# Performance work log

Measured on AMD Instinct MI355X. Metric: run time of the kernel, lower is better.

## Reference

```python
import jax, jax.numpy as jnp
import numpy as np

B, C, H, W_SP = 4, 64, 64, 64
CI = C // 2  # inter_channels = 32
DEPTH = 64
EPS = 1e-5


def conv2d(x, w, b, pad=0, dil=1):
    out = jax.lax.conv_general_dilated(
        x, w, window_strides=(1, 1),
        padding=[(pad, pad), (pad, pad)],
        rhs_dilation=(dil, dil),
        dimension_numbers=('NCHW', 'OIHW', 'NCHW'))
    return out + b[None, :, None, None]


def setup_inputs() -> dict:
    key = jax.random.key(0)
    ks = iter(jax.random.split(key, 32))
    nrm = lambda shp, s=0.01: jax.random.normal(next(ks), shp, jnp.float32) * s
    inp = {
        'x': jax.random.normal(next(ks), (B, C, H, W_SP), jnp.float32),
        # NonlocalBlock params (init: normal(0, 0.01), bias 0)
        'g_w': nrm((CI, C, 1, 1)), 'g_b': jnp.zeros((CI,), jnp.float32),
        'theta_w': nrm((CI, C, 1, 1)), 'theta_b': jnp.zeros((CI,), jnp.float32),
        'phi_w': nrm((CI, C, 1, 1)), 'phi_b': jnp.zeros((CI,), jnp.float32),
        'Wz_w': nrm((C, CI, 1, 1)), 'Wz_b': jnp.zeros((C,), jnp.float32),
        'bn_g': jax.random.normal(next(ks), (C,), jnp.float32),  # normal_(W[1].weight, 0) -> std 1
        'bn_b': jnp.zeros((C,), jnp.float32),
        # ASPP params (torch default kaiming init approximated by small normals)
        'a_mean_w': nrm((DEPTH, C, 1, 1), 0.05), 'a_mean_b': jnp.zeros((DEPTH,), jnp.float32),
        'a1_w': nrm((DEPTH, C, 1, 1), 0.05), 'a1_b': jnp.zeros((DEPTH,), jnp.float32),
        'a3_w': nrm((DEPTH, C, 3, 3), 0.02), 'a3_b': jnp.zeros((DEPTH,), jnp.float32),
        'a5_w': nrm((DEPTH, C, 3, 3), 0.02), 'a5_b': jnp.zeros((DEPTH,), jnp.float32),
        'a7_w': nrm((DEPTH, C, 3, 3), 0.02), 'a7_b': jnp.zeros((DEPTH,), jnp.float32),
        'out_w': nrm((DEPTH, DEPTH * 5, 1, 1), 0.02), 'out_b': jnp.zeros((DEPTH,), jnp.float32),
    }
    return inp


def _forward(x, g_w, g_b, theta_w, theta_b, phi_w, phi_b, Wz_w, Wz_b, bn_g, bn_b,
             a_mean_w, a_mean_b, a1_w, a1_b, a3_w, a3_b, a5_w, a5_b, a7_w, a7_b,
             out_w, out_b):
    b, c, h, w = x.shape
    n = h * w
    # ---- NonlocalBlock: global self-attention ----
    g_x = conv2d(x, g_w, g_b).reshape(b, CI, n).transpose(0, 2, 1)       # [B,N,Ci]
    theta_x = conv2d(x, theta_w, theta_b).reshape(b, CI, n).transpose(0, 2, 1)  # [B,N,Ci]
    phi_x = conv2d(x, phi_w, phi_b).reshape(b, CI, n)                    # [B,Ci,N]
    f = jnp.einsum('bqc,bck->bqk', theta_x, phi_x)                       # [B,N,N]
    f_div_C = jax.nn.softmax(f, axis=2)
    y = jnp.einsum('bqk,bkc->bqc', f_div_C, g_x)                         # [B,N,Ci]
    y = y.transpose(0, 2, 1).reshape(b, CI, h, w)
    wy = conv2d(y, Wz_w, Wz_b)
    # BatchNorm (eval: running_mean=0, running_var=1)
    wy = wy * (bn_g / jnp.sqrt(1.0 + EPS))[None, :, None, None] + bn_b[None, :, None, None]
    z = wy + x
    # ---- ASPP ----
    img = jnp.mean(z, axis=(2, 3), keepdims=True)                        # [B,C,1,1]
    img = conv2d(img, a_mean_w, a_mean_b)                                # [B,D,1,1]
    img = jnp.broadcast_to(img, (b, DEPTH, h, w))  # bilinear upsample of 1x1 is constant
    b1 = conv2d(z, a1_w, a1_b)
    b3 = conv2d(z, a3_w, a3_b, pad=3, dil=3)
    b5 = conv2d(z, a5_w, a5_b, pad=5, dil=5)
    b7 = conv2d(z, a7_w, a7_b, pad=7, dil=7)
    cat = jnp.concatenate([img, b1, b3, b5, b7], axis=1)                 # [B,5D,H,W]
    return conv2d(cat, out_w, out_b)                                     # [B,D,H,W]


def reference(x, g_w, g_b, theta_w, theta_b, phi_w, phi_b, Wz_w, Wz_b, bn_g, bn_b,
              a_mean_w, a_mean_b, a1_w, a1_b, a3_w, a3_b, a5_w, a5_b, a7_w, a7_b,
              out_w, out_b):
    return _forward(x, g_w, g_b, theta_w, theta_b, phi_w, phi_b, Wz_w, Wz_b, bn_g, bn_b,
                    a_mean_w, a_mean_b, a1_w, a1_b, a3_w, a3_b, a5_w, a5_b, a7_w, a7_b,
                    out_w, out_b)
```

## Files before the change

### kernel.cpp

```cpp
#include <hip/hip_runtime.h>


typedef __attribute__((ext_vector_type(8))) short bf16x8;
typedef __attribute__((ext_vector_type(4))) short s16x4;
typedef __attribute__((ext_vector_type(4))) float f32x4;

#define MFMA(a, b, c) __builtin_amdgcn_mfma_f32_16x16x32_bf16((a), (b), (c), 0, 0, 0)

#if __has_builtin(__builtin_amdgcn_exp2f)
#define EXP2(x) __builtin_amdgcn_exp2f(x)
#else
#define EXP2(x) exp2f(x)
#endif

__device__ static inline short f2bf(float f) {
  union { float f; unsigned u; } v; v.f = f;
  unsigned r = v.u + 0x7fffu + ((v.u >> 16) & 1u);
  return (short)(r >> 16);
}
__device__ static inline s16x4 pk4(f32x4 v) {
  s16x4 r; r.x = f2bf(v.x); r.y = f2bf(v.y); r.z = f2bf(v.z); r.w = f2bf(v.w);
  return r;
}
__device__ static inline unsigned pk2(float f0, float f1) {
  union { float f; unsigned u; } a, b; a.f = f0; b.f = f1;
  return __builtin_amdgcn_perm(b.u, a.u, 0x07060302u);
}
__device__ static inline float unlo(unsigned d) {
  union { unsigned u; float f; } v; v.u = d << 16; return v.f;
}
__device__ static inline float unhi(unsigned d) {
  union { unsigned u; float f; } v; v.u = d & 0xffff0000u; return v.f;
}
__device__ static inline unsigned fasu(float f) {
  union { float f; unsigned u; } v; v.f = f; return v.u;
}
__device__ static inline float uasf(unsigned u) {
  union { unsigned u; float f; } v; v.u = u; return v.f;
}
__device__ static inline f32x4 exp24(f32x4 v) {
  f32x4 r; r.x = EXP2(v.x); r.y = EXP2(v.y); r.z = EXP2(v.z); r.w = EXP2(v.w);
  return r;
}

#define QF_PER_B 131072
#define ZPB      389376
#define LOG2E    1.4426950408889634f

__global__ __launch_bounds__(256) void k_proj(
    const float* __restrict__ x,
    const float* __restrict__ tw, const float* __restrict__ tb,
    const float* __restrict__ pw, const float* __restrict__ pb,
    const float* __restrict__ gw, const float* __restrict__ gb,
    const float* __restrict__ Wz_w, const float* __restrict__ Wz_b,
    const float* __restrict__ bn_g, const float* __restrict__ bn_b,
    const float* __restrict__ out_w, const float* __restrict__ out_b,
    const float* __restrict__ a1_w, const float* __restrict__ a3_w,
    const float* __restrict__ a5_w, const float* __restrict__ a7_w,
    const float* __restrict__ a1_b, const float* __restrict__ a3_b,
    const float* __restrict__ a5_b, const float* __restrict__ a7_b,
    const float* __restrict__ am_w,
    unsigned short* __restrict__ thetaB, unsigned short* __restrict__ phiB,
    unsigned short* __restrict__ gB, unsigned short* __restrict__ WzF,
    float* __restrict__ bias2, float* __restrict__ zmean,
    unsigned* __restrict__ zp, unsigned short* __restrict__ Wfrag,
    float* __restrict__ am_wT, float* __restrict__ owT0,
    float* __restrict__ cbias) {
  __shared__ union {
    struct { float wl[2048]; float bl[32]; } qkv;
    struct { float wsm[4096]; float osm[64 * 65]; } prep;
  } sm;
  int blk = blockIdx.x, t = threadIdx.x;
  if (blk < 192) {
    int b = blk & 3, pt = (blk >> 2) & 15, proj = blk >> 6;
    const float* w    = proj == 0 ? tw : (proj == 1 ? pw : gw);
    const float* bias = proj == 0 ? tb : (proj == 1 ? pb : gb);
    for (int i = t; i < 2048; i += 256) sm.qkv.wl[i] = w[i];
    if (t < 32) sm.qkv.bl[t] = bias[t];
    __syncthreads();
    int pix = pt*256 + t;
    const float* xp = x + b*64*4096 + pix;
    float acc[32];
    #pragma unroll
    for (int ci = 0; ci < 32; ++ci) acc[ci] = sm.qkv.bl[ci];
    for (int c0 = 0; c0 < 64; c0 += 16) {
      float xv[16];
      #pragma unroll
      for (int k = 0; k < 16; ++k) xv[k] = xp[(c0 + k)*4096];
      #pragma unroll
      for (int k = 0; k < 16; ++k)
        #pragma unroll
        for (int ci = 0; ci < 32; ++ci) acc[ci] += sm.qkv.wl[ci*64 + c0 + k] * xv[k];
    }
    if (proj == 0) {
      #pragma unroll
      for (int ci = 0; ci < 32; ++ci) acc[ci] *= LOG2E;
    }
    if (proj < 2) {
      unsigned short* base = (proj == 0 ? thetaB : phiB) + b*QF_PER_B
                             + (pix >> 4)*512 + (pix & 15)*8;
      #pragma unroll
      for (int q = 0; q < 4; ++q) {
        bf16x8 v;
        #pragma unroll
        for (int j = 0; j < 8; ++j) v[j] = f2bf(acc[q*8 + j]);
        *(bf16x8*)(base + q*128) = v;
      }
    } else {
      unsigned short* base = gB + b*QF_PER_B + (pix >> 5)*1024
                             + ((pix & 31) >> 3)*128 + (pix & 7);
      #pragma unroll
      for (int ci = 0; ci < 32; ++ci)
        base[(ci >> 4)*512 + (ci & 15)*8] = (unsigned short)f2bf(acc[ci]);
    }
  } else if (blk == 192) {
    int ct = t >> 6, lane = t & 63, quad = lane >> 4, l15 = lane & 15;
    int c = ct * 16 + l15;
    float s = bn_g[c] * rsqrtf(1.f + 1e-5f);
    bf16x8 v;
    #pragma unroll
    for (int j = 0; j < 8; ++j) v[j] = f2bf(s * Wz_w[c * 32 + quad * 8 + j]);
    *(bf16x8*)(WzF + (ct * 64 + lane) * 8) = v;
    zmean[t] = 0.f;
    if (t < 64) {
      float s2 = bn_g[t] * rsqrtf(1.f + 1e-5f);
      bias2[t] = s2 * Wz_b[t] + bn_b[t];
    }
  } else if (blk < 1189) {
    int hb = blk - 193;
    int b = hb / 249, loc = hb - b * 249;
    int i = loc * 256 + t;
    if (i >= 63616) return;
    int px = i >> 5, dw = i & 31;
    int row, col;
    if (px < 1092) {
      int r = px / 78; col = px - r * 78;
      row = (r < 7) ? r : r + 64;
    } else {
      int j = px - 1092;
      int r = j / 14; int c = j - r * 14;
      row = r + 7; col = (c < 7) ? c : c + 64;
    }
    zp[b * (ZPB / 2) + (row * 78 + col) * 32 + dw] = 0u;
  } else if (blk < 1217) {
    int tap = blk - 1189;
    const float* w; int goff, kyx = 0, ksq = 9;
    if (tap == 0)      { w = a1_w; goff = 64;  ksq = 1; }
    else if (tap < 10) { w = a3_w; goff = 128; kyx = tap - 1; }
    else if (tap < 19) { w = a5_w; goff = 192; kyx = tap - 10; }
    else               { w = a7_w; goff = 256; kyx = tap - 19; }
    for (int i = t; i < 4096; i += 256) {
      sm.prep.wsm[i] = w[i * ksq + kyx];
      int d = i >> 6, m = i & 63;
      sm.prep.osm[d * 65 + m] = out_w[d * 320 + goff + m];
    }
    __syncthreads();
    int dt = t >> 6, lane = t & 63, quad = lane >> 4, l15 = lane & 15;
    int d = dt * 16 + l15;
    float acc[16];
    #pragma unroll
    for (int k = 0; k < 16; ++k) acc[k] = 0.f;
    const float* orow = sm.prep.osm + d * 65;
    int c0 = quad * 8;
    for (int m = 0; m < 64; ++m) {
      float o = orow[m];
      const float* wr = sm.prep.wsm + m * 64 + c0;
      #pragma unroll
      for (int cc = 0; cc < 2; ++cc)
        #pragma unroll
        for (int j = 0; j < 8; ++j)
          acc[cc * 8 + j] += o * wr[cc * 32 + j];
    }
    #pragma unroll
    for (int cc = 0; cc < 2; ++cc) {
      bf16x8 v;
      #pragma unroll
      for (int j = 0; j < 8; ++j) v[j] = f2bf(acc[cc * 8 + j]);
      *(bf16x8*)(Wfrag + (((tap * 4 + dt) * 2 + cc) * 64 + lane) * 8) = v;
    }
  } else {
    for (int i = t; i < 4096; i += 256) {
      int d = i >> 6, c = i & 63;
      am_wT[c * 64 + d] = am_w[i];
      owT0[c * 64 + d] = out_w[d * 320 + c];
    }
    if (t < 64) {
      float r = out_b[t];
      const float* ow = out_w + t * 320;
      for (int m = 0; m < 64; ++m)
        r += ow[64 + m] * a1_b[m] + ow[128 + m] * a3_b[m]
           + ow[192 + m] * a5_b[m] + ow[256 + m] * a7_b[m];
      cbias[t] = r;
    }
  }
}

__global__ __launch_bounds__(512, 4) void k_attn(
    const unsigned short* __restrict__ thetaB, const unsigned short* __restrict__ phiB,
    const unsigned short* __restrict__ gB, const unsigned short* __restrict__ WzF,
    const float* __restrict__ bias2, const float* __restrict__ x,
    unsigned short* __restrict__ z_pad, float* __restrict__ zmean) {
  __shared__ struct {
    unsigned ypk[8][10][64];
    __align__(16) unsigned short plds[8][1152];
  } sm;
  int blk = blockIdx.x;
  int b = blk >> 7, qblk = blk & 127;
  int tid = threadIdx.x;
  int kh = tid >> 6, lane = tid & 63, quad = lane >> 4, l15 = lane & 15;
  const bf16x8* thB = (const bf16x8*)(thetaB + b*QF_PER_B);
  const bf16x8* phF = (const bf16x8*)(phiB + b*QF_PER_B);
  const bf16x8* gF  = (const bf16x8*)(gB + b*QF_PER_B);
  bf16x8 th0 = thB[(qblk*2 + 0)*64 + lane];
  bf16x8 th1 = thB[(qblk*2 + 1)*64 + lane];
  bf16x8 ones;
  #pragma unroll
  for (int j = 0; j < 8; ++j) ones[j] = (short)0x3F80;
  const f32x4 z4 = {0.f, 0.f, 0.f, 0.f};
  f32x4 acc00 = z4, acc01 = z4, acc10 = z4, acc11 = z4;
  f32x4 accL0 = z4, accL1 = z4;
  unsigned short* pl = &sm.plds[kh][0];
  unsigned short* r0p = pl + l15*36 + quad*4;
  unsigned short* r1p = pl + 576 + l15*36 + quad*4;
  const unsigned short* q0p = pl + l15*36 + quad*8;
  const unsigned short* q1p = pl + 576 + l15*36 + quad*8;
  int kt0 = kh*16;
  int tb0 = kt0*128 + lane;
  bf16x8 pf0 = phF[tb0], pf1 = phF[tb0 + 64];
  bf16x8 gf0 = gF[tb0],  gf1 = gF[tb0 + 64];
  for (int kt = kt0; kt < kt0 + 16; ++kt) {
    bf16x8 cp0 = pf0, cp1 = pf1, cg0 = gf0, cg1 = gf1;
    if (kt + 1 < kt0 + 16) {
      int tb = (kt + 1)*128 + lane;
      pf0 = phF[tb]; pf1 = phF[tb + 64];
      gf0 = gF[tb];  gf1 = gF[tb + 64];
    }
    f32x4 s00 = MFMA(cp0, th0, z4);
    f32x4 s10 = MFMA(cp1, th0, z4);
    f32x4 s01 = MFMA(cp0, th1, z4);
    f32x4 s11 = MFMA(cp1, th1, z4);
    f32x4 p00 = exp24(s00), p10 = exp24(s10), p01 = exp24(s01), p11 = exp24(s11);
    uint2 w0; w0.x = pk2(p00.x, p00.y); w0.y = pk2(p00.z, p00.w);
    uint2 w1; w1.x = pk2(p10.x, p10.y); w1.y = pk2(p10.z, p10.w);
    uint2 w2; w2.x = pk2(p01.x, p01.y); w2.y = pk2(p01.z, p01.w);
    uint2 w3; w3.x = pk2(p11.x, p11.y); w3.y = pk2(p11.z, p11.w);
    *(uint2*)(r0p)      = w0;
    *(uint2*)(r0p + 16) = w1;
    *(uint2*)(r1p)      = w2;
    *(uint2*)(r1p + 16) = w3;
    uint2 a0 = *(const uint2*)(q0p);
    uint2 a1 = *(const uint2*)(q0p + 4);
    uint2 b0 = *(const uint2*)(q1p);
    uint2 b1 = *(const uint2*)(q1p + 4);
    union { unsigned u[4]; bf16x8 v; } pb0c, pb1c;
    pb0c.u[0] = a0.x; pb0c.u[1] = a0.y; pb0c.u[2] = a1.x; pb0c.u[3] = a1.y;
    pb1c.u[0] = b0.x; pb1c.u[1] = b0.y; pb1c.u[2] = b1.x; pb1c.u[3] = b1.y;
    acc00 = MFMA(cg0, pb0c.v, acc00);
    acc01 = MFMA(cg1, pb0c.v, acc01);
    acc10 = MFMA(cg0, pb1c.v, acc10);
    acc11 = MFMA(cg1, pb1c.v, acc11);
    accL0 = MFMA(ones, pb0c.v, accL0);
    accL1 = MFMA(ones, pb1c.v, accL1);
  }
  {
    unsigned* yp = &sm.ypk[kh][0][lane];
    yp[0*64] = pk2(acc00.x, acc00.y);
    yp[1*64] = pk2(acc00.z, acc00.w);
    yp[2*64] = pk2(acc01.x, acc01.y);
    yp[3*64] = pk2(acc01.z, acc01.w);
    yp[4*64] = pk2(acc10.x, acc10.y);
    yp[5*64] = pk2(acc10.z, acc10.w);
    yp[6*64] = pk2(acc11.x, acc11.y);
    yp[7*64] = pk2(acc11.z, acc11.w);
    yp[8*64] = fasu(accL0.x);
    yp[9*64] = fasu(accL1.x);
  }
  __syncthreads();
  if (kh >= 4) return;
  int ct = kh;
  f32x4 a00 = z4, a01 = z4, a10 = z4, a11 = z4;
  float l0 = 0.f, l1 = 0.f;
  #pragma unroll
  for (int k = 0; k < 8; ++k) {
    const unsigned* q = &sm.ypk[k][0][lane];
    unsigned d0v = q[0], d1v = q[64], d2v = q[128], d3v = q[192];
    unsigned d4v = q[256], d5v = q[320], d6v = q[384], d7v = q[448];
    a00.x += unlo(d0v); a00.y += unhi(d0v); a00.z += unlo(d1v); a00.w += unhi(d1v);
    a01.x += unlo(d2v); a01.y += unhi(d2v); a01.z += unlo(d3v); a01.w += unhi(d3v);
    a10.x += unlo(d4v); a10.y += unhi(d4v); a10.z += unlo(d5v); a10.w += unhi(d5v);
    a11.x += unlo(d6v); a11.y += unhi(d6v); a11.z += unlo(d7v); a11.w += unhi(d7v);
    l0 += uasf(q[512]); l1 += uasf(q[576]);
  }
  float r0 = 1.f / l0, r1 = 1.f / l1;
  a00 *= r0; a01 *= r0; a10 *= r1; a11 *= r1;
  unsigned short* yl = &sm.plds[0][0] + ct*1280;
  *(s16x4*)(yl + l15*40 + quad*4)             = pk4(a00);
  *(s16x4*)(yl + l15*40 + 16 + quad*4)        = pk4(a01);
  *(s16x4*)(yl + (16 + l15)*40 + quad*4)      = pk4(a10);
  *(s16x4*)(yl + (16 + l15)*40 + 16 + quad*4) = pk4(a11);
  bf16x8 y0 = *(const bf16x8*)(yl + l15*40 + quad*8);
  bf16x8 y1 = *(const bf16x8*)(yl + (16 + l15)*40 + quad*8);
  bf16x8 wf = ((const bf16x8*)WzF)[ct*64 + lane];
  f32x4 zq0 = MFMA(wf, y0, z4);
  f32x4 zq1 = MFMA(wf, y1, z4);
  int c0 = ct*16 + quad*4;
  f32x4 b2 = *(const f32x4*)(bias2 + c0);
  int q0i = qblk * 32;
  const float* xp0 = x + (b*64 + c0)*4096 + q0i + l15;
  f32x4 s0, s1;
  s0.x = zq0.x + b2.x + xp0[0];
  s0.y = zq0.y + b2.y + xp0[4096];
  s0.z = zq0.z + b2.z + xp0[8192];
  s0.w = zq0.w + b2.w + xp0[12288];
  s1.x = zq1.x + b2.x + xp0[16];
  s1.y = zq1.y + b2.y + xp0[4096 + 16];
  s1.z = zq1.z + b2.z + xp0[8192 + 16];
  s1.w = zq1.w + b2.w + xp0[12288 + 16];
  {
    int q = q0i + l15, h = q >> 6, w = q & 63;
    *(s16x4*)(z_pad + b*ZPB + ((h + 7)*78 + (w + 7))*64 + c0) = pk4(s0);
    q = q0i + 16 + l15; h = q >> 6; w = q & 63;
    *(s16x4*)(z_pad + b*ZPB + ((h + 7)*78 + (w + 7))*64 + c0) = pk4(s1);
  }
  f32x4 zs = s0 + s1;
  #pragma unroll
  for (int m = 1; m < 16; m <<= 1) {
    zs.x += __shfl_xor(zs.x, m);
    zs.y += __shfl_xor(zs.y, m);
    zs.z += __shfl_xor(zs.z, m);
    zs.w += __shfl_xor(zs.w, m);
  }
  if (l15 == 0) {
    atomicAdd(zmean + b*64 + c0 + 0, zs.x);
    atomicAdd(zmean + b*64 + c0 + 1, zs.y);
    atomicAdd(zmean + b*64 + c0 + 2, zs.z);
    atomicAdd(zmean + b*64 + c0 + 3, zs.w);
  }
}

__global__ __launch_bounds__(256, 4) void k_conv(
    const unsigned short* __restrict__ z_pad, const unsigned short* __restrict__ Wfrag,
    const float* __restrict__ zmean, const float* __restrict__ am_wT,
    const float* __restrict__ am_b, const float* __restrict__ owT0,
    const float* __restrict__ cbias, float* __restrict__ out) {
  static constexpr int DYt[28] = {0, -3,-3,-3,0,0,0,3,3,3,
                                     -5,-5,-5,0,0,0,5,5,5,
                                     -7,-7,-7,0,0,0,7,7,7};
  static constexpr int DXt[28] = {0, -3,0,3,-3,0,3,-3,0,3,
                                     -5,0,5,-5,0,5,-5,0,5,
                                     -7,0,7,-7,0,7,-7,0,7};
  int blk = blockIdx.x;
  int b = blk >> 6, h = blk & 63;
  int tid = threadIdx.x;
  int wave = tid >> 6, lane = tid & 63, quad = lane >> 4, l15 = lane & 15;
  int dt2 = wave >> 1, wt2 = wave & 1;
  float zml = zmean[b*64 + lane] * (1.f / 4096.f);
  float img = am_b[lane];
  for (int c = 0; c < 64; ++c) img += am_wT[c*64 + lane] * __shfl(zml, c);
  float cbd = cbias[lane];
  for (int dd = 0; dd < 64; ++dd) cbd += owT0[dd*64 + lane] * __shfl(img, dd);
  const unsigned short* zb = z_pad + b*ZPB + ((h + 7)*78 + 7)*64 + quad*8;
  const bf16x8* wfp = (const bf16x8*)Wfrag + lane;
  int d0 = dt2*2 + 0, d1 = dt2*2 + 1;
  const f32x4 z4 = {0.f, 0.f, 0.f, 0.f};
  f32x4 acc00 = z4, acc01 = z4, acc10 = z4, acc11 = z4;
  int col0 = ((wt2*2 + 0)*16 + l15)*64;
  int col1 = ((wt2*2 + 1)*16 + l15)*64;
  bf16x8 zq0[4], zq1[4], wq0[4], wq1[4];
  #pragma unroll
  for (int p = 0; p < 4; ++p) {
    int tap = p >> 1, cc = p & 1;
    const unsigned short* nz = zb + (DYt[tap]*78 + DXt[tap])*64 + cc*32;
    zq0[p] = *(const bf16x8*)(nz + col0);
    zq1[p] = *(const bf16x8*)(nz + col1);
    wq0[p] = wfp[((tap*4 + d0)*2 + cc)*64];
    wq1[p] = wfp[((tap*4 + d1)*2 + cc)*64];
  }
  #pragma unroll
  for (int idx = 0; idx < 56; ++idx) {
    int slot = idx & 3;
    bf16x8 zc0 = zq0[slot], zc1 = zq1[slot], wc0 = wq0[slot], wc1 = wq1[slot];
    if (idx + 4 < 56) {
      int ntap = (idx + 4) >> 1, ncc = (idx + 4) & 1;
      const unsigned short* nz = zb + (DYt[ntap]*78 + DXt[ntap])*64 + ncc*32;
      zq0[slot] = *(const bf16x8*)(nz + col0);
      zq1[slot] = *(const bf16x8*)(nz + col1);
      wq0[slot] = wfp[((ntap*4 + d0)*2 + ncc)*64];
      wq1[slot] = wfp[((ntap*4 + d1)*2 + ncc)*64];
    }
    acc00 = MFMA(wc0, zc0, acc00);
    acc01 = MFMA(wc0, zc1, acc01);
    acc10 = MFMA(wc1, zc0, acc10);
    acc11 = MFMA(wc1, zc1, acc11);
  }
  int dd0 = d0*16 + quad*4, dd1 = d1*16 + quad*4;
  f32x4 cb0v, cb1v;
  cb0v.x = __shfl(cbd, dd0 + 0); cb0v.y = __shfl(cbd, dd0 + 1);
  cb0v.z = __shfl(cbd, dd0 + 2); cb0v.w = __shfl(cbd, dd0 + 3);
  cb1v.x = __shfl(cbd, dd1 + 0); cb1v.y = __shfl(cbd, dd1 + 1);
  cb1v.z = __shfl(cbd, dd1 + 2); cb1v.w = __shfl(cbd, dd1 + 3);
  acc00 += cb0v; acc01 += cb0v; acc10 += cb1v; acc11 += cb1v;
  float* ob = out + b*262144 + h*64;
  int w0 = (wt2*2 + 0)*16 + l15, w1 = (wt2*2 + 1)*16 + l15;
  ob[(dd0 + 0)*4096 + w0] = acc00.x;
  ob[(dd0 + 1)*4096 + w0] = acc00.y;
  ob[(dd0 + 2)*4096 + w0] = acc00.z;
  ob[(dd0 + 3)*4096 + w0] = acc00.w;
  ob[(dd0 + 0)*4096 + w1] = acc01.x;
  ob[(dd0 + 1)*4096 + w1] = acc01.y;
  ob[(dd0 + 2)*4096 + w1] = acc01.z;
  ob[(dd0 + 3)*4096 + w1] = acc01.w;
  ob[(dd1 + 0)*4096 + w0] = acc10.x;
  ob[(dd1 + 1)*4096 + w0] = acc10.y;
  ob[(dd1 + 2)*4096 + w0] = acc10.z;
  ob[(dd1 + 3)*4096 + w0] = acc10.w;
  ob[(dd1 + 0)*4096 + w1] = acc11.x;
  ob[(dd1 + 1)*4096 + w1] = acc11.y;
  ob[(dd1 + 2)*4096 + w1] = acc11.z;
  ob[(dd1 + 3)*4096 + w1] = acc11.w;
}

extern "C" void kernel_launch(void* const* d_in, const int* in_sizes, int n_in,
                              void* d_out, int out_size, void* d_ws, size_t ws_size,
                              hipStream_t stream) {
  const float* x    = (const float*)d_in[0];
  const float* g_w  = (const float*)d_in[1];
  const float* g_b  = (const float*)d_in[2];
  const float* th_w = (const float*)d_in[3];
  const float* th_b = (const float*)d_in[4];
  const float* ph_w = (const float*)d_in[5];
  const float* ph_b = (const float*)d_in[6];
  const float* Wz_w = (const float*)d_in[7];
  const float* Wz_b = (const float*)d_in[8];
  const float* bn_g = (const float*)d_in[9];
  const float* bn_b = (const float*)d_in[10];
  const float* am_w = (const float*)d_in[11];
  const float* am_b = (const float*)d_in[12];
  const float* a1_w = (const float*)d_in[13];
  const float* a1_b = (const float*)d_in[14];
  const float* a3_w = (const float*)d_in[15];
  const float* a3_b = (const float*)d_in[16];
  const float* a5_w = (const float*)d_in[17];
  const float* a5_b = (const float*)d_in[18];
  const float* a7_w = (const float*)d_in[19];
  const float* a7_b = (const float*)d_in[20];
  const float* out_w = (const float*)d_in[21];
  const float* out_b = (const float*)d_in[22];
  float* out = (float*)d_out;
  char* ws = (char*)d_ws;
  unsigned short* thetaB = (unsigned short*)(ws + 0);
  unsigned short* phiB   = (unsigned short*)(ws + 1048576);
  unsigned short* gB     = (unsigned short*)(ws + 2097152);
  unsigned short* z_pad  = (unsigned short*)(ws + 3145728);
  unsigned short* Wfrag  = (unsigned short*)(ws + 6260736);
  unsigned short* WzF    = (unsigned short*)(ws + 6490112);
  float* zmean           = (float*)(ws + 6494208);
  float* bias2           = (float*)(ws + 6495232);
  float* am_wT           = (float*)(ws + 6495488);
  float* owT0            = (float*)(ws + 6511872);
  float* cbias           = (float*)(ws + 6528256);

  k_proj<<<dim3(1218), dim3(256), 0, stream>>>(
      x, th_w, th_b, ph_w, ph_b, g_w, g_b, Wz_w, Wz_b, bn_g, bn_b,
      out_w, out_b, a1_w, a3_w, a5_w, a7_w, a1_b, a3_b, a5_b, a7_b, am_w,
      thetaB, phiB, gB, WzF, bias2, zmean,
      (unsigned*)z_pad, Wfrag, am_wT, owT0, cbias);
  k_attn<<<dim3(512), dim3(512), 0, stream>>>(thetaB, phiB, gB, WzF, bias2, x,
                                              z_pad, zmean);
  k_conv<<<dim3(256), dim3(256), 0, stream>>>(z_pad, Wfrag, zmean, am_wT, am_b,
                                              owT0, cbias, out);
}
```

Before: 180.7 us.

## Halve per-block work across all three kernels and add XCD-aware block mapping

Doubles the grid of each kernel by splitting work. The projection kernel splits output channels across two thread halves and reads weights from LDS as transposed vector loads. Attention handles 16 queries per block with launch bounds raised to 8, and conv handles 32 columns per block. Attention and conv blocks are remapped so blocks on the same XCD share a batch or rows for L2 locality. The z-mean accumulation is spread over 8 partial buffers to reduce atomic contention. The trade-off is less register reuse per block: theta and weights are reloaded more often, and gB loads are no longer prefetched.

```diff
diff --git a/kernel.cpp b/kernel.cpp
--- a/kernel.cpp
+++ b/kernel.cpp
@@ -62,58 +62,68 @@
     const float* __restrict__ am_w,
     unsigned short* __restrict__ thetaB, unsigned short* __restrict__ phiB,
     unsigned short* __restrict__ gB, unsigned short* __restrict__ WzF,
-    float* __restrict__ bias2, float* __restrict__ zmean,
+    float* __restrict__ bias2, float* __restrict__ zpart,
     unsigned* __restrict__ zp, unsigned short* __restrict__ Wfrag,
     float* __restrict__ am_wT, float* __restrict__ owT0,
     float* __restrict__ cbias) {
   __shared__ union {
-    struct { float wl[2048]; float bl[32]; } qkv;
+    struct { float wlT[2048]; float bl[32]; } qkv;
     struct { float wsm[4096]; float osm[64 * 65]; } prep;
   } sm;
   int blk = blockIdx.x, t = threadIdx.x;
-  if (blk < 192) {
-    int b = blk & 3, pt = (blk >> 2) & 15, proj = blk >> 6;
+  if (blk < 384) {
+    int proj = blk >> 7, r = blk & 127;
+    int b = r & 3, pt = r >> 2;
     const float* w    = proj == 0 ? tw : (proj == 1 ? pw : gw);
     const float* bias = proj == 0 ? tb : (proj == 1 ? pb : gb);
-    for (int i = t; i < 2048; i += 256) sm.qkv.wl[i] = w[i];
+    for (int i = t; i < 2048; i += 256)
+      sm.qkv.wlT[(i & 63) * 32 + (i >> 6)] = w[i];
     if (t < 32) sm.qkv.bl[t] = bias[t];
     __syncthreads();
-    int pix = pt*256 + t;
-    const float* xp = x + b*64*4096 + pix;
-    float acc[32];
+    int px = pt * 128 + (t & 127), tci = t >> 7;
+    const float* xp = x + b*64*4096 + px;
+    float acc[16];
     #pragma unroll
-    for (int ci = 0; ci < 32; ++ci) acc[ci] = sm.qkv.bl[ci];
+    for (int i = 0; i < 16; ++i) acc[i] = sm.qkv.bl[tci*16 + i];
     for (int c0 = 0; c0 < 64; c0 += 16) {
       float xv[16];
       #pragma unroll
       for (int k = 0; k < 16; ++k) xv[k] = xp[(c0 + k)*4096];
       #pragma unroll
-      for (int k = 0; k < 16; ++k)
+      for (int k = 0; k < 16; ++k) {
+        const float* wr = &sm.qkv.wlT[(c0 + k)*32 + tci*16];
         #pragma unroll
-        for (int ci = 0; ci < 32; ++ci) acc[ci] += sm.qkv.wl[ci*64 + c0 + k] * xv[k];
+        for (int j = 0; j < 4; ++j) {
+          f32x4 wv = *(const f32x4*)(wr + j*4);
+          acc[j*4 + 0] += wv.x * xv[k];
+          acc[j*4 + 1] += wv.y * xv[k];
+          acc[j*4 + 2] += wv.z * xv[k];
+          acc[j*4 + 3] += wv.w * xv[k];
+        }
+      }
     }
     if (proj == 0) {
       #pragma unroll
-      for (int ci = 0; ci < 32; ++ci) acc[ci] *= LOG2E;
+      for (int i = 0; i < 16; ++i) acc[i] *= LOG2E;
     }
     if (proj < 2) {
       unsigned short* base = (proj == 0 ? thetaB : phiB) + b*QF_PER_B
-                             + (pix >> 4)*512 + (pix & 15)*8;
-      #pragma unroll
-      for (int q = 0; q < 4; ++q) {
+                             + (px >> 4)*512 + (px & 15)*8;
+      #pragma unroll
+      for (int qq = 0; qq < 2; ++qq) {
         bf16x8 v;
         #pragma unroll
-        for (int j = 0; j < 8; ++j) v[j] = f2bf(acc[q*8 + j]);
-        *(bf16x8*)(base + q*128) = v;
+        for (int j = 0; j < 8; ++j) v[j] = f2bf(acc[qq*8 + j]);
+        *(bf16x8*)(base + (tci*2 + qq)*128) = v;
       }
     } else {
-      unsigned short* base = gB + b*QF_PER_B + (pix >> 5)*1024
-                             + ((pix & 31) >> 3)*128 + (pix & 7);
-      #pragma unroll
-      for (int ci = 0; ci < 32; ++ci)
-        base[(ci >> 4)*512 + (ci & 15)*8] = (unsigned short)f2bf(acc[ci]);
-    }
-  } else if (blk == 192) {
+      unsigned short* base = gB + b*QF_PER_B + (px >> 5)*1024
+                             + ((px & 31) >> 3)*128 + (px & 7) + tci*512;
+      #pragma unroll
+      for (int ci = 0; ci < 16; ++ci)
+        base[ci*8] = (unsigned short)f2bf(acc[ci]);
+    }
+  } else if (blk == 384) {
     int ct = t >> 6, lane = t & 63, quad = lane >> 4, l15 = lane & 15;
     int c = ct * 16 + l15;
     float s = bn_g[c] * rsqrtf(1.f + 1e-5f);
@@ -121,13 +131,14 @@
     #pragma unroll
     for (int j = 0; j < 8; ++j) v[j] = f2bf(s * Wz_w[c * 32 + quad * 8 + j]);
     *(bf16x8*)(WzF + (ct * 64 + lane) * 8) = v;
-    zmean[t] = 0.f;
+    #pragma unroll
+    for (int i = 0; i < 8; ++i) zpart[i*256 + t] = 0.f;
     if (t < 64) {
       float s2 = bn_g[t] * rsqrtf(1.f + 1e-5f);
       bias2[t] = s2 * Wz_b[t] + bn_b[t];
     }
-  } else if (blk < 1189) {
-    int hb = blk - 193;
+  } else if (blk < 1381) {
+    int hb = blk - 385;
     int b = hb / 249, loc = hb - b * 249;
     int i = loc * 256 + t;
     if (i >= 63616) return;
@@ -142,8 +153,8 @@
       row = r + 7; col = (c < 7) ? c : c + 64;
     }
     zp[b * (ZPB / 2) + (row * 78 + col) * 32 + dw] = 0u;
-  } else if (blk < 1217) {
-    int tap = blk - 1189;
+  } else if (blk < 1409) {
+    int tap = blk - 1381;
     const float* w; int goff, kyx = 0, ksq = 9;
     if (tap == 0)      { w = a1_w; goff = 64;  ksq = 1; }
     else if (tap < 10) { w = a3_w; goff = 128; kyx = tap - 1; }
@@ -195,134 +206,100 @@
   }
 }
 
-__global__ __launch_bounds__(512, 4) void k_attn(
+__global__ __launch_bounds__(512, 8) void k_attn(
     const unsigned short* __restrict__ thetaB, const unsigned short* __restrict__ phiB,
     const unsigned short* __restrict__ gB, const unsigned short* __restrict__ WzF,
     const float* __restrict__ bias2, const float* __restrict__ x,
-    unsigned short* __restrict__ z_pad, float* __restrict__ zmean) {
+    unsigned short* __restrict__ z_pad, float* __restrict__ zpart) {
   __shared__ struct {
-    unsigned ypk[8][10][64];
-    __align__(16) unsigned short plds[8][1152];
+    unsigned ypk[8][5][64];
+    __align__(16) unsigned short plds[8][576];
   } sm;
   int blk = blockIdx.x;
-  int b = blk >> 7, qblk = blk & 127;
+  int xcd = blk & 7;
+  int b = xcd >> 1;
+  int qblk = ((xcd & 1) << 7) | (blk >> 3);
   int tid = threadIdx.x;
   int kh = tid >> 6, lane = tid & 63, quad = lane >> 4, l15 = lane & 15;
   const bf16x8* thB = (const bf16x8*)(thetaB + b*QF_PER_B);
   const bf16x8* phF = (const bf16x8*)(phiB + b*QF_PER_B);
   const bf16x8* gF  = (const bf16x8*)(gB + b*QF_PER_B);
-  bf16x8 th0 = thB[(qblk*2 + 0)*64 + lane];
-  bf16x8 th1 = thB[(qblk*2 + 1)*64 + lane];
+  bf16x8 th = thB[qblk*64 + lane];
   bf16x8 ones;
   #pragma unroll
   for (int j = 0; j < 8; ++j) ones[j] = (short)0x3F80;
   const f32x4 z4 = {0.f, 0.f, 0.f, 0.f};
-  f32x4 acc00 = z4, acc01 = z4, acc10 = z4, acc11 = z4;
-  f32x4 accL0 = z4, accL1 = z4;
+  f32x4 acc0 = z4, acc1 = z4, accL = z4;
   unsigned short* pl = &sm.plds[kh][0];
-  unsigned short* r0p = pl + l15*36 + quad*4;
-  unsigned short* r1p = pl + 576 + l15*36 + quad*4;
-  const unsigned short* q0p = pl + l15*36 + quad*8;
-  const unsigned short* q1p = pl + 576 + l15*36 + quad*8;
+  unsigned short* rp = pl + l15*36 + quad*4;
+  const unsigned short* qp = pl + l15*36 + quad*8;
   int kt0 = kh*16;
   int tb0 = kt0*128 + lane;
   bf16x8 pf0 = phF[tb0], pf1 = phF[tb0 + 64];
-  bf16x8 gf0 = gF[tb0],  gf1 = gF[tb0 + 64];
   for (int kt = kt0; kt < kt0 + 16; ++kt) {
-    bf16x8 cp0 = pf0, cp1 = pf1, cg0 = gf0, cg1 = gf1;
+    bf16x8 cp0 = pf0, cp1 = pf1;
+    bf16x8 gf0 = gF[kt*128 + lane];
+    bf16x8 gf1 = gF[kt*128 + lane + 64];
     if (kt + 1 < kt0 + 16) {
       int tb = (kt + 1)*128 + lane;
       pf0 = phF[tb]; pf1 = phF[tb + 64];
-      gf0 = gF[tb];  gf1 = gF[tb + 64];
-    }
-    f32x4 s00 = MFMA(cp0, th0, z4);
-    f32x4 s10 = MFMA(cp1, th0, z4);
-    f32x4 s01 = MFMA(cp0, th1, z4);
-    f32x4 s11 = MFMA(cp1, th1, z4);
-    f32x4 p00 = exp24(s00), p10 = exp24(s10), p01 = exp24(s01), p11 = exp24(s11);
-    uint2 w0; w0.x = pk2(p00.x, p00.y); w0.y = pk2(p00.z, p00.w);
-    uint2 w1; w1.x = pk2(p10.x, p10.y); w1.y = pk2(p10.z, p10.w);
-    uint2 w2; w2.x = pk2(p01.x, p01.y); w2.y = pk2(p01.z, p01.w);
-    uint2 w3; w3.x = pk2(p11.x, p11.y); w3.y = pk2(p11.z, p11.w);
-    *(uint2*)(r0p)      = w0;
-    *(uint2*)(r0p + 16) = w1;
-    *(uint2*)(r1p)      = w2;
-    *(uint2*)(r1p + 16) = w3;
-    uint2 a0 = *(const uint2*)(q0p);
-    uint2 a1 = *(const uint2*)(q0p + 4);
-    uint2 b0 = *(const uint2*)(q1p);
-    uint2 b1 = *(const uint2*)(q1p + 4);
-    union { unsigned u[4]; bf16x8 v; } pb0c, pb1c;
-    pb0c.u[0] = a0.x; pb0c.u[1] = a0.y; pb0c.u[2] = a1.x; pb0c.u[3] = a1.y;
-    pb1c.u[0] = b0.x; pb1c.u[1] = b0.y; pb1c.u[2] = b1.x; pb1c.u[3] = b1.y;
-    acc00 = MFMA(cg0, pb0c.v, acc00);
-    acc01 = MFMA(cg1, pb0c.v, acc01);
-    acc10 = MFMA(cg0, pb1c.v, acc10);
-    acc11 = MFMA(cg1, pb1c.v, acc11);
-    accL0 = MFMA(ones, pb0c.v, accL0);
-    accL1 = MFMA(ones, pb1c.v, accL1);
+    }
+    f32x4 s0 = MFMA(cp0, th, z4);
+    f32x4 s1 = MFMA(cp1, th, z4);
+    f32x4 p0 = exp24(s0), p1 = exp24(s1);
+    uint2 w0; w0.x = pk2(p0.x, p0.y); w0.y = pk2(p0.z, p0.w);
+    uint2 w1; w1.x = pk2(p1.x, p1.y); w1.y = pk2(p1.z, p1.w);
+    *(uint2*)(rp)      = w0;
+    *(uint2*)(rp + 16) = w1;
+    uint2 a0 = *(const uint2*)(qp);
+    uint2 a1 = *(const uint2*)(qp + 4);
+    union { unsigned u[4]; bf16x8 v; } pb;
+    pb.u[0] = a0.x; pb.u[1] = a0.y; pb.u[2] = a1.x; pb.u[3] = a1.y;
+    acc0 = MFMA(gf0, pb.v, acc0);
+    acc1 = MFMA(gf1, pb.v, acc1);
+    accL = MFMA(ones, pb.v, accL);
   }
   {
     unsigned* yp = &sm.ypk[kh][0][lane];
-    yp[0*64] = pk2(acc00.x, acc00.y);
-    yp[1*64] = pk2(acc00.z, acc00.w);
-    yp[2*64] = pk2(acc01.x, acc01.y);
-    yp[3*64] = pk2(acc01.z, acc01.w);
-    yp[4*64] = pk2(acc10.x, acc10.y);
-    yp[5*64] = pk2(acc10.z, acc10.w);
-    yp[6*64] = pk2(acc11.x, acc11.y);
-    yp[7*64] = pk2(acc11.z, acc11.w);
-    yp[8*64] = fasu(accL0.x);
-    yp[9*64] = fasu(accL1.x);
+    yp[0*64] = pk2(acc0.x, acc0.y);
+    yp[1*64] = pk2(acc0.z, acc0.w);
+    yp[2*64] = pk2(acc1.x, acc1.y);
+    yp[3*64] = pk2(acc1.z, acc1.w);
+    yp[4*64] = fasu(accL.x);
   }
   __syncthreads();
   if (kh >= 4) return;
   int ct = kh;
-  f32x4 a00 = z4, a01 = z4, a10 = z4, a11 = z4;
-  float l0 = 0.f, l1 = 0.f;
+  f32x4 a0 = z4, a1 = z4;
+  float l = 0.f;
   #pragma unroll
   for (int k = 0; k < 8; ++k) {
     const unsigned* q = &sm.ypk[k][0][lane];
     unsigned d0v = q[0], d1v = q[64], d2v = q[128], d3v = q[192];
-    unsigned d4v = q[256], d5v = q[320], d6v = q[384], d7v = q[448];
-    a00.x += unlo(d0v); a00.y += unhi(d0v); a00.z += unlo(d1v); a00.w += unhi(d1v);
-    a01.x += unlo(d2v); a01.y += unhi(d2v); a01.z += unlo(d3v); a01.w += unhi(d3v);
-    a10.x += unlo(d4v); a10.y += unhi(d4v); a10.z += unlo(d5v); a10.w += unhi(d5v);
-    a11.x += unlo(d6v); a11.y += unhi(d6v); a11.z += unlo(d7v); a11.w += unhi(d7v);
-    l0 += uasf(q[512]); l1 += uasf(q[576]);
-  }
-  float r0 = 1.f / l0, r1 = 1.f / l1;
-  a00 *= r0; a01 *= r0; a10 *= r1; a11 *= r1;
-  unsigned short* yl = &sm.plds[0][0] + ct*1280;
-  *(s16x4*)(yl + l15*40 + quad*4)             = pk4(a00);
-  *(s16x4*)(yl + l15*40 + 16 + quad*4)        = pk4(a01);
-  *(s16x4*)(yl + (16 + l15)*40 + quad*4)      = pk4(a10);
-  *(s16x4*)(yl + (16 + l15)*40 + 16 + quad*4) = pk4(a11);
-  bf16x8 y0 = *(const bf16x8*)(yl + l15*40 + quad*8);
-  bf16x8 y1 = *(const bf16x8*)(yl + (16 + l15)*40 + quad*8);
+    a0.x += unlo(d0v); a0.y += unhi(d0v); a0.z += unlo(d1v); a0.w += unhi(d1v);
+    a1.x += unlo(d2v); a1.y += unhi(d2v); a1.z += unlo(d3v); a1.w += unhi(d3v);
+    l += uasf(q[256]);
+  }
+  float rl = 1.f / l;
+  a0 *= rl; a1 *= rl;
+  unsigned short* yl = &sm.plds[ct][0];
+  *(s16x4*)(yl + l15*36 + quad*4)      = pk4(a0);
+  *(s16x4*)(yl + l15*36 + 16 + quad*4) = pk4(a1);
+  bf16x8 y = *(const bf16x8*)(yl + l15*36 + quad*8);
   bf16x8 wf = ((const bf16x8*)WzF)[ct*64 + lane];
-  f32x4 zq0 = MFMA(wf, y0, z4);
-  f32x4 zq1 = MFMA(wf, y1, z4);
+  f32x4 zq = MFMA(wf, y, z4);
   int c0 = ct*16 + quad*4;
   f32x4 b2 = *(const f32x4*)(bias2 + c0);
-  int q0i = qblk * 32;
-  const float* xp0 = x + (b*64 + c0)*4096 + q0i + l15;
-  f32x4 s0, s1;
-  s0.x = zq0.x + b2.x + xp0[0];
-  s0.y = zq0.y + b2.y + xp0[4096];
-  s0.z = zq0.z + b2.z + xp0[8192];
-  s0.w = zq0.w + b2.w + xp0[12288];
-  s1.x = zq1.x + b2.x + xp0[16];
-  s1.y = zq1.y + b2.y + xp0[4096 + 16];
-  s1.z = zq1.z + b2.z + xp0[8192 + 16];
-  s1.w = zq1.w + b2.w + xp0[12288 + 16];
-  {
-    int q = q0i + l15, h = q >> 6, w = q & 63;
-    *(s16x4*)(z_pad + b*ZPB + ((h + 7)*78 + (w + 7))*64 + c0) = pk4(s0);
-    q = q0i + 16 + l15; h = q >> 6; w = q & 63;
-    *(s16x4*)(z_pad + b*ZPB + ((h + 7)*78 + (w + 7))*64 + c0) = pk4(s1);
-  }
-  f32x4 zs = s0 + s1;
+  int q = qblk*16 + l15;
+  const float* xp = x + (b*64 + c0)*4096 + q;
+  f32x4 s;
+  s.x = zq.x + b2.x + xp[0];
+  s.y = zq.y + b2.y + xp[4096];
+  s.z = zq.z + b2.z + xp[8192];
+  s.w = zq.w + b2.w + xp[12288];
+  int h = q >> 6, w = q & 63;
+  *(s16x4*)(z_pad + b*ZPB + ((h + 7)*78 + (w + 7))*64 + c0) = pk4(s);
+  f32x4 zs = s;
   #pragma unroll
   for (int m = 1; m < 16; m <<= 1) {
     zs.x += __shfl_xor(zs.x, m);
@@ -331,16 +308,17 @@
     zs.w += __shfl_xor(zs.w, m);
   }
   if (l15 == 0) {
-    atomicAdd(zmean + b*64 + c0 + 0, zs.x);
-    atomicAdd(zmean + b*64 + c0 + 1, zs.y);
-    atomicAdd(zmean + b*64 + c0 + 2, zs.z);
-    atomicAdd(zmean + b*64 + c0 + 3, zs.w);
+    float* zd = zpart + (qblk & 7)*256 + b*64 + c0;
+    atomicAdd(zd + 0, zs.x);
+    atomicAdd(zd + 1, zs.y);
+    atomicAdd(zd + 2, zs.z);
+    atomicAdd(zd + 3, zs.w);
   }
 }
 
 __global__ __launch_bounds__(256, 4) void k_conv(
     const unsigned short* __restrict__ z_pad, const unsigned short* __restrict__ Wfrag,
-    const float* __restrict__ zmean, const float* __restrict__ am_wT,
+    const float* __restrict__ zpart, const float* __restrict__ am_wT,
     const float* __restrict__ am_b, const float* __restrict__ owT0,
     const float* __restrict__ cbias, float* __restrict__ out) {
   static constexpr int DYt[28] = {0, -3,-3,-3,0,0,0,3,3,3,
@@ -350,11 +328,17 @@
                                      -5,0,5,-5,0,5,-5,0,5,
                                      -7,0,7,-7,0,7,-7,0,7};
   int blk = blockIdx.x;
-  int b = blk >> 6, h = blk & 63;
+  int xcd = blk & 7, idx = blk >> 3;
+  int h = xcd*8 + (idx & 7);
+  int rest = idx >> 3;
+  int b = rest & 3, wh = rest >> 2;
   int tid = threadIdx.x;
   int wave = tid >> 6, lane = tid & 63, quad = lane >> 4, l15 = lane & 15;
-  int dt2 = wave >> 1, wt2 = wave & 1;
-  float zml = zmean[b*64 + lane] * (1.f / 4096.f);
+  int dt2 = wave >> 1, cf = wave & 1;
+  float zm = 0.f;
+  #pragma unroll
+  for (int p = 0; p < 8; ++p) zm += zpart[p*256 + b*64 + lane];
+  float zml = zm * (1.f / 4096.f);
   float img = am_b[lane];
   for (int c = 0; c < 64; ++c) img += am_wT[c*64 + lane] * __shfl(zml, c);
   float cbd = cbias[lane];
@@ -363,35 +347,28 @@
   const bf16x8* wfp = (const bf16x8*)Wfrag + lane;
   int d0 = dt2*2 + 0, d1 = dt2*2 + 1;
   const f32x4 z4 = {0.f, 0.f, 0.f, 0.f};
-  f32x4 acc00 = z4, acc01 = z4, acc10 = z4, acc11 = z4;
-  int col0 = ((wt2*2 + 0)*16 + l15)*64;
-  int col1 = ((wt2*2 + 1)*16 + l15)*64;
-  bf16x8 zq0[4], zq1[4], wq0[4], wq1[4];
+  f32x4 acc0 = z4, acc1 = z4;
+  int col = ((wh*2 + cf)*16 + l15)*64;
+  bf16x8 zq[4], wq0[4], wq1[4];
   #pragma unroll
   for (int p = 0; p < 4; ++p) {
     int tap = p >> 1, cc = p & 1;
-    const unsigned short* nz = zb + (DYt[tap]*78 + DXt[tap])*64 + cc*32;
-    zq0[p] = *(const bf16x8*)(nz + col0);
-    zq1[p] = *(const bf16x8*)(nz + col1);
+    zq[p] = *(const bf16x8*)(zb + (DYt[tap]*78 + DXt[tap])*64 + cc*32 + col);
     wq0[p] = wfp[((tap*4 + d0)*2 + cc)*64];
     wq1[p] = wfp[((tap*4 + d1)*2 + cc)*64];
   }
   #pragma unroll
-  for (int idx = 0; idx < 56; ++idx) {
-    int slot = idx & 3;
-    bf16x8 zc0 = zq0[slot], zc1 = zq1[slot], wc0 = wq0[slot], wc1 = wq1[slot];
-    if (idx + 4 < 56) {
-      int ntap = (idx + 4) >> 1, ncc = (idx + 4) & 1;
-      const unsigned short* nz = zb + (DYt[ntap]*78 + DXt[ntap])*64 + ncc*32;
-      zq0[slot] = *(const bf16x8*)(nz + col0);
-      zq1[slot] = *(const bf16x8*)(nz + col1);
+  for (int idx2 = 0; idx2 < 56; ++idx2) {
+    int slot = idx2 & 3;
+    bf16x8 zc = zq[slot], wc0 = wq0[slot], wc1 = wq1[slot];
+    if (idx2 + 4 < 56) {
+      int ntap = (idx2 + 4) >> 1, ncc = (idx2 + 4) & 1;
+      zq[slot] = *(const bf16x8*)(zb + (DYt[ntap]*78 + DXt[ntap])*64 + ncc*32 + col);
       wq0[slot] = wfp[((ntap*4 + d0)*2 + ncc)*64];
       wq1[slot] = wfp[((ntap*4 + d1)*2 + ncc)*64];
     }
-    acc00 = MFMA(wc0, zc0, acc00);
-    acc01 = MFMA(wc0, zc1, acc01);
-    acc10 = MFMA(wc1, zc0, acc10);
-    acc11 = MFMA(wc1, zc1, acc11);
+    acc0 = MFMA(wc0, zc, acc0);
+    acc1 = MFMA(wc1, zc, acc1);
   }
   int dd0 = d0*16 + quad*4, dd1 = d1*16 + quad*4;
   f32x4 cb0v, cb1v;
@@ -399,25 +376,17 @@
   cb0v.z = __shfl(cbd, dd0 + 2); cb0v.w = __shfl(cbd, dd0 + 3);
   cb1v.x = __shfl(cbd, dd1 + 0); cb1v.y = __shfl(cbd, dd1 + 1);
   cb1v.z = __shfl(cbd, dd1 + 2); cb1v.w = __shfl(cbd, dd1 + 3);
-  acc00 += cb0v; acc01 += cb0v; acc10 += cb1v; acc11 += cb1v;
+  acc0 += cb0v; acc1 += cb1v;
   float* ob = out + b*262144 + h*64;
-  int w0 = (wt2*2 + 0)*16 + l15, w1 = (wt2*2 + 1)*16 + l15;
-  ob[(dd0 + 0)*4096 + w0] = acc00.x;
-  ob[(dd0 + 1)*4096 + w0] = acc00.y;
-  ob[(dd0 + 2)*4096 + w0] = acc00.z;
-  ob[(dd0 + 3)*4096 + w0] = acc00.w;
-  ob[(dd0 + 0)*4096 + w1] = acc01.x;
-  ob[(dd0 + 1)*4096 + w1] = acc01.y;
-  ob[(dd0 + 2)*4096 + w1] = acc01.z;
-  ob[(dd0 + 3)*4096 + w1] = acc01.w;
-  ob[(dd1 + 0)*4096 + w0] = acc10.x;
-  ob[(dd1 + 1)*4096 + w0] = acc10.y;
-  ob[(dd1 + 2)*4096 + w0] = acc10.z;
-  ob[(dd1 + 3)*4096 + w0] = acc10.w;
-  ob[(dd1 + 0)*4096 + w1] = acc11.x;
-  ob[(dd1 + 1)*4096 + w1] = acc11.y;
-  ob[(dd1 + 2)*4096 + w1] = acc11.z;
-  ob[(dd1 + 3)*4096 + w1] = acc11.w;
+  int w0 = (wh*2 + cf)*16 + l15;
+  ob[(dd0 + 0)*4096 + w0] = acc0.x;
+  ob[(dd0 + 1)*4096 + w0] = acc0.y;
+  ob[(dd0 + 2)*4096 + w0] = acc0.z;
+  ob[(dd0 + 3)*4096 + w0] = acc0.w;
+  ob[(dd1 + 0)*4096 + w0] = acc1.x;
+  ob[(dd1 + 1)*4096 + w0] = acc1.y;
+  ob[(dd1 + 2)*4096 + w0] = acc1.z;
+  ob[(dd1 + 3)*4096 + w0] = acc1.w;
 }
 
 extern "C" void kernel_launch(void* const* d_in, const int* in_sizes, int n_in,
@@ -454,19 +423,19 @@
   unsigned short* z_pad  = (unsigned short*)(ws + 3145728);
   unsigned short* Wfrag  = (unsigned short*)(ws + 6260736);
   unsigned short* WzF    = (unsigned short*)(ws + 6490112);
-  float* zmean           = (float*)(ws + 6494208);
   float* bias2           = (float*)(ws + 6495232);
   float* am_wT           = (float*)(ws + 6495488);
   float* owT0            = (float*)(ws + 6511872);
   float* cbias           = (float*)(ws + 6528256);
-
-  k_proj<<<dim3(1218), dim3(256), 0, stream>>>(
+  float* zpart           = (float*)(ws + 6528512);
+
+  k_proj<<<dim3(1410), dim3(256), 0, stream>>>(
       x, th_w, th_b, ph_w, ph_b, g_w, g_b, Wz_w, Wz_b, bn_g, bn_b,
       out_w, out_b, a1_w, a3_w, a5_w, a7_w, a1_b, a3_b, a5_b, a7_b, am_w,
-      thetaB, phiB, gB, WzF, bias2, zmean,
+      thetaB, phiB, gB, WzF, bias2, zpart,
       (unsigned*)z_pad, Wfrag, am_wT, owT0, cbias);
-  k_attn<<<dim3(512), dim3(512), 0, stream>>>(thetaB, phiB, gB, WzF, bias2, x,
-                                              z_pad, zmean);
-  k_conv<<<dim3(256), dim3(256), 0, stream>>>(z_pad, Wfrag, zmean, am_wT, am_b,
+  k_attn<<<dim3(1024), dim3(512), 0, stream>>>(thetaB, phiB, gB, WzF, bias2, x,
+                                               z_pad, zpart);
+  k_conv<<<dim3(512), dim3(256), 0, stream>>>(z_pad, Wfrag, zpart, am_wT, am_b,
                                               owT0, cbias, out);
 }
```

Measured after the change: 162.5 us. 10.1% less time.
